# Kernel optimization log

Hardware: AMD Instinct MI355X
Metric: run time of the kernel (lower is better)

## Reference

```python
import jax, jax.numpy as jnp
import numpy as np

IN_FEAT = 256
HIDDEN = [512, 512]
DENSE = 512
BATCH, SEQ = 64, 1024


def setup_inputs() -> dict:
    key = jax.random.key(0)
    ks = jax.random.split(key, 16)
    d = {"x": jax.random.normal(ks[0], (BATCH, SEQ, IN_FEAT), dtype=jnp.float32)}
    in_dim = IN_FEAT
    ki = 1
    for li, h in enumerate(HIDDEN):
        # packed input kernel [in,3h] (r,z,n), input bias [3h], packed hidden kernel [h,3h], hn bias [h]
        d[f"W_i{li}"] = jax.random.normal(ks[ki], (in_dim, 3 * h), dtype=jnp.float32) / np.sqrt(in_dim); ki += 1
        d[f"b_i{li}"] = jnp.zeros((3 * h,), dtype=jnp.float32)
        d[f"W_h{li}"] = jax.random.normal(ks[ki], (h, 3 * h), dtype=jnp.float32) / np.sqrt(h); ki += 1
        d[f"b_hn{li}"] = jnp.zeros((h,), dtype=jnp.float32)
        in_dim = h
    d["W_out"] = jax.random.normal(ks[ki], (in_dim, DENSE), dtype=jnp.float32) / np.sqrt(in_dim)
    d["b_out"] = jnp.zeros((DENSE,), dtype=jnp.float32)
    return d


def _gru_layer(x, W_i, b_i, W_h, b_hn):
    """x: [B,T,D]. Flax GRUCell math: r,z gates sigmoid; n tanh with r-gated hidden path (hn has its own bias)."""
    B, T, _ = x.shape
    H = W_h.shape[0]
    # precompute all input-side gate projections once: [B,T,3H]
    xg = jnp.einsum('btd,dg->btg', x, W_i) + b_i

    def step(h, xg_t):
        hg = h @ W_h                              # [B,3H]
        xr, xz, xn = jnp.split(xg_t, 3, axis=-1)
        hr, hz, hn = jnp.split(hg, 3, axis=-1)
        r = jax.nn.sigmoid(xr + hr)
        z = jax.nn.sigmoid(xz + hz)
        n = jnp.tanh(xn + r * (hn + b_hn))
        h_new = (1.0 - z) * n + z * h
        return h_new, h_new

    h0 = jnp.zeros((B, H), x.dtype)
    hT, ys = jax.lax.scan(step, h0, jnp.swapaxes(xg, 0, 1))  # ys: [T,B,H]
    return hT, jnp.swapaxes(ys, 0, 1)


def reference(x, W_i0, b_i0, W_h0, b_hn0, W_i1, b_i1, W_h1, b_hn1, W_out, b_out):
    act = jnp.tanh
    c0, y = _gru_layer(x, W_i0, b_i0, W_h0, b_hn0)
    y = act(y)
    c1, y = _gru_layer(y, W_i1, b_i1, W_h1, b_hn1)
    y = act(y)
    out = act(y[:, -1, :] @ W_out + b_out)
    return (out, c0, c1)
```

## Files before the change

kernel.cpp:

```cpp
#include <hip/hip_runtime.h>


#define T_STEPS 1024
#define NWG_L0  32
#define NWG_TOT 64

typedef _Float16 f16x8 __attribute__((ext_vector_type(8)));
typedef float    f32x4 __attribute__((ext_vector_type(4)));

#define H0_OFF   0
#define H1_OFF   131072
#define Y0_OFF   262144
#define FLAG_OFF 393216
#define FSTRIDE  32

#define BUD_BAR  (1ull << 22)

#define WAITV0()   asm volatile("s_waitcnt vmcnt(0)")
#define SB()       __builtin_amdgcn_sched_barrier(0)
#define FENCE_VM() asm volatile("s_waitcnt vmcnt(0)" ::: "memory")

__device__ __forceinline__ float sigm_f(float x) { return 1.0f / (1.0f + __expf(-x)); }
__device__ __forceinline__ float tanh_f(float x) { return 2.0f / (1.0f + __expf(-2.0f * x)) - 1.0f; }

__device__ __forceinline__ f32x4 mfma16(f16x8 a, f16x8 b, f32x4 c) {
    return __builtin_amdgcn_mfma_f32_16x16x32_f16(a, b, c, 0, 0, 0);
}

__device__ __forceinline__ f16x8 pack8(const float* __restrict__ src, int stride) {
    f16x8 r;
#pragma unroll
    for (int j = 0; j < 8; ++j) r[j] = (_Float16)src[j * stride];
    return r;
}

__device__ __forceinline__ f16x8 ld_frag_a(const _Float16* p) {
    f16x8 v;
    asm volatile("global_load_dwordx4 %0, %1, off sc1" : "=v"(v) : "v"(p));
    return v;
}

__device__ __forceinline__ void st_dev_f16(_Float16* p, float v) {
    unsigned short b = __builtin_bit_cast(unsigned short, (_Float16)v);
    __hip_atomic_store((unsigned short*)p, b, __ATOMIC_RELAXED, __HIP_MEMORY_SCOPE_AGENT);
}

__device__ __forceinline__ void bar_arrive(unsigned* flags, int wg, unsigned epoch) {
    asm volatile("s_waitcnt vmcnt(0)" ::: "memory");
    __syncthreads();
    if (threadIdx.x == 0)
        __hip_atomic_store(&flags[wg * FSTRIDE], epoch,
                           __ATOMIC_RELAXED, __HIP_MEMORY_SCOPE_AGENT);
}
__device__ __forceinline__ void bar_wait_wd(const unsigned* flags, unsigned epoch,
                                            int wave, int lane,
                                            volatile unsigned* s_alive) {
    if (wave == 0 && *s_alive) {
        const unsigned* p = &flags[lane * FSTRIDE];
        unsigned long long t0 = clock64();
        for (;;) {
            unsigned v = __hip_atomic_load(p, __ATOMIC_RELAXED, __HIP_MEMORY_SCOPE_AGENT);
            if (__all(v >= epoch)) break;
            if (clock64() - t0 > BUD_BAR) { if (lane == 0) *s_alive = 0; break; }
        }
    }
    __syncthreads();
    asm volatile("" ::: "memory");
}

#define BFRAG(g, kt) __builtin_bit_cast(f16x8, ldsB[((g) * 16 + (kt)) * 64 + lane])

__global__ __launch_bounds__(256, 1) void gru_scan(
    const float* __restrict__ x,
    const float* __restrict__ Wi0,
    const float* __restrict__ bi0,
    const float* __restrict__ Wh0,
    const float* __restrict__ bhn0,
    const float* __restrict__ Wi1,
    const float* __restrict__ bi1,
    const float* __restrict__ Wh1,
    const float* __restrict__ bhn1,
    float* __restrict__ c0_out,
    float* __restrict__ c1_out,
    unsigned char* __restrict__ ws)
{
    __shared__ uint4 ldsB[48 * 64];
    __shared__ unsigned s_alive;

    const int tid  = threadIdx.x;
    const int wave = tid >> 6;
    const int lane = tid & 63;
    const int quad = lane >> 4;
    const int l16  = lane & 15;
    const int wg   = blockIdx.x;
    const bool isL1 = (wg >= NWG_L0);
    const int cslice = (isL1 ? (wg - NWG_L0) : wg) * 16;

    if (tid == 0) s_alive = 1u;

    _Float16* h0buf = (_Float16*)(ws + H0_OFF);
    _Float16* h1buf = (_Float16*)(ws + H1_OFF);
    _Float16* y0buf = (_Float16*)(ws + Y0_OFF);
    unsigned* flags = (unsigned*)(ws + FLAG_OFF);

    const float* Wh = isL1 ? Wh1 : Wh0;
    const float* Wi = isL1 ? Wi1 : Wi0;

    for (int f = wave * 12; f < wave * 12 + 12; ++f) {
        int nt = f >> 4, kt = f & 15;
        const float* src = Wh + (kt * 32 + quad * 8) * 1536 + nt * 512 + cslice + l16;
        ldsB[f * 64 + lane] = __builtin_bit_cast(uint4, pack8(src, 1536));
    }

    f16x8 wif[48];
    if (!isL1) {
#pragma unroll
        for (int nt = 0; nt < 3; ++nt)
#pragma unroll
            for (int kt = 0; kt < 8; ++kt)
                wif[nt * 8 + kt] = pack8(Wi + (kt * 32 + quad * 8) * 1536 + nt * 512 + cslice + l16, 1536);
    } else {
#pragma unroll
        for (int nt = 0; nt < 3; ++nt)
#pragma unroll
            for (int kt = 0; kt < 16; ++kt)
                wif[nt * 16 + kt] = pack8(Wi + (kt * 32 + quad * 8) * 1536 + nt * 512 + cslice + l16, 1536);
    }

    const float* bi = isL1 ? bi1 : bi0;
    const float* bh = isL1 ? bhn1 : bhn0;
    const float bi_r = bi[cslice + l16];
    const float bi_z = bi[512 + cslice + l16];
    const float bi_n = bi[1024 + cslice + l16];
    const float bhn  = bh[cslice + l16];

    __syncthreads();

    float hstate[4] = {0.f, 0.f, 0.f, 0.f};
    const int rowA = wave * 16 + l16;
    const int rowC = wave * 16 + quad * 4;
    const int cu   = cslice + l16;
    const f32x4 z4 = {0.f, 0.f, 0.f, 0.f};

    for (int s = 0; s < T_STEPS + 1; ++s) {
        const int pr = s & 1;

        f32x4 xr[16];
        if (!isL1 && s < T_STEPS) {
            const float* px = x + (size_t)rowA * 262144 + s * 256 + quad * 8;
#pragma unroll
            for (int kt = 0; kt < 8; ++kt) {
                xr[kt * 2]     = *(const f32x4*)(px + kt * 32);
                xr[kt * 2 + 1] = *(const f32x4*)(px + kt * 32 + 4);
            }
        }

        if (s > 0) bar_wait_wd(flags, (unsigned)s, wave, lane, &s_alive);

        if (!isL1 && s < T_STEPS) {
            const _Float16* hR = h0buf + pr * 32768;
            _Float16* hW = h0buf + (pr ^ 1) * 32768;
            _Float16* yW = y0buf + (pr ^ 1) * 32768;

            FENCE_VM();

            f16x8 axf[8];
#pragma unroll
            for (int kt = 0; kt < 8; ++kt) {
                f32x4 x0 = xr[kt * 2], x1 = xr[kt * 2 + 1];
                f16x8 a;
                a[0] = (_Float16)x0[0]; a[1] = (_Float16)x0[1];
                a[2] = (_Float16)x0[2]; a[3] = (_Float16)x0[3];
                a[4] = (_Float16)x1[0]; a[5] = (_Float16)x1[1];
                a[6] = (_Float16)x1[2]; a[7] = (_Float16)x1[3];
                axf[kt] = a;
            }
            SB();

            f16x8 hb[16];
#pragma unroll
            for (int p = 0; p < 16; ++p)
                hb[p] = ld_frag_a(hR + rowA * 512 + p * 32 + quad * 8);

            f32x4 ax0 = z4, ax1 = z4, ax2 = z4;
#pragma unroll
            for (int kt = 0; kt < 8; ++kt) {
                ax0 = mfma16(axf[kt], wif[0 * 8 + kt], ax0);
                ax1 = mfma16(axf[kt], wif[1 * 8 + kt], ax1);
                ax2 = mfma16(axf[kt], wif[2 * 8 + kt], ax2);
            }

            SB(); WAITV0(); SB();

            f32x4 ah0 = z4, ah1 = z4, ah2 = z4;
#pragma unroll
            for (int kt = 0; kt < 16; ++kt) {
                f16x8 a = hb[kt];
                ah0 = mfma16(a, BFRAG(0, kt), ah0);
                ah1 = mfma16(a, BFRAG(1, kt), ah1);
                ah2 = mfma16(a, BFRAG(2, kt), ah2);
            }

#pragma unroll
            for (int i = 0; i < 4; ++i) {
                const int b = rowC + i;
                float r = sigm_f(ax0[i] + bi_r + ah0[i]);
                float z = sigm_f(ax1[i] + bi_z + ah1[i]);
                float n = tanh_f(ax2[i] + bi_n + r * (ah2[i] + bhn));
                float hnew = (1.0f - z) * n + z * hstate[i];
                hstate[i] = hnew;
                st_dev_f16(&hW[b * 512 + cu], hnew);
                st_dev_f16(&yW[b * 512 + cu], tanh_f(hnew));
                if (s == T_STEPS - 1) c0_out[b * 512 + cu] = hnew;
            }
        }

        if (isL1 && s >= 1) {
            const _Float16* hR = h1buf + pr * 32768;
            _Float16* hW = h1buf + (pr ^ 1) * 32768;
            const _Float16* yR = y0buf + pr * 32768;

            FENCE_VM();
            SB();

            f16x8 hb[8], yb[8];
#pragma unroll
            for (int p = 0; p < 8; ++p) {
                hb[p] = ld_frag_a(hR + rowA * 512 + p * 32 + quad * 8);
                yb[p] = ld_frag_a(yR + rowA * 512 + p * 32 + quad * 8);
            }

            SB(); WAITV0(); SB();

            f32x4 ah0 = z4, ah1 = z4, ah2 = z4, ax0 = z4, ax1 = z4, ax2 = z4;
#pragma unroll
            for (int kt = 0; kt < 8; ++kt) {
                f16x8 ah = hb[kt], ay = yb[kt];
                ah0 = mfma16(ah, BFRAG(0, kt), ah0);
                ah1 = mfma16(ah, BFRAG(1, kt), ah1);
                ah2 = mfma16(ah, BFRAG(2, kt), ah2);
                ax0 = mfma16(ay, wif[0 * 16 + kt], ax0);
                ax1 = mfma16(ay, wif[1 * 16 + kt], ax1);
                ax2 = mfma16(ay, wif[2 * 16 + kt], ax2);
                hb[kt] = ld_frag_a(hR + rowA * 512 + (kt + 8) * 32 + quad * 8);
                yb[kt] = ld_frag_a(yR + rowA * 512 + (kt + 8) * 32 + quad * 8);
            }

            SB(); WAITV0(); SB();

#pragma unroll
            for (int kt = 8; kt < 16; ++kt) {
                f16x8 ah = hb[kt - 8], ay = yb[kt - 8];
                ah0 = mfma16(ah, BFRAG(0, kt), ah0);
                ah1 = mfma16(ah, BFRAG(1, kt), ah1);
                ah2 = mfma16(ah, BFRAG(2, kt), ah2);
                ax0 = mfma16(ay, wif[0 * 16 + kt], ax0);
                ax1 = mfma16(ay, wif[1 * 16 + kt], ax1);
                ax2 = mfma16(ay, wif[2 * 16 + kt], ax2);
            }

#pragma unroll
            for (int i = 0; i < 4; ++i) {
                const int b = rowC + i;
                float r = sigm_f(ax0[i] + bi_r + ah0[i]);
                float z = sigm_f(ax1[i] + bi_z + ah1[i]);
                float n = tanh_f(ax2[i] + bi_n + r * (ah2[i] + bhn));
                float hnew = (1.0f - z) * n + z * hstate[i];
                hstate[i] = hnew;
                st_dev_f16(&hW[b * 512 + cu], hnew);
                if (s == T_STEPS) c1_out[b * 512 + cu] = hnew;
            }
        }

        if (s < T_STEPS) bar_arrive(flags, wg, (unsigned)(s + 1));
    }
}

__global__ __launch_bounds__(256) void dense_out(
    const float* __restrict__ c1, const float* __restrict__ Wout,
    const float* __restrict__ bout, float* __restrict__ out)
{
    __shared__ float a[512];
    const int b = blockIdx.x, tid = threadIdx.x;
    a[tid]       = tanh_f(c1[b * 512 + tid]);
    a[tid + 256] = tanh_f(c1[b * 512 + tid + 256]);
    __syncthreads();
    float acc0 = 0.f, acc1 = 0.f;
#pragma unroll 4
    for (int k = 0; k < 512; ++k) {
        const float av = a[k];
        acc0 += av * Wout[k * 512 + tid];
        acc1 += av * Wout[k * 512 + tid + 256];
    }
    out[b * 512 + tid]       = tanh_f(acc0 + bout[tid]);
    out[b * 512 + tid + 256] = tanh_f(acc1 + bout[tid + 256]);
}

extern "C" void kernel_launch(void* const* d_in, const int* in_sizes, int n_in,
                              void* d_out, int out_size, void* d_ws, size_t ws_size,
                              hipStream_t stream)
{
    const float* x    = (const float*)d_in[0];
    const float* Wi0  = (const float*)d_in[1];
    const float* bi0  = (const float*)d_in[2];
    const float* Wh0  = (const float*)d_in[3];
    const float* bhn0 = (const float*)d_in[4];
    const float* Wi1  = (const float*)d_in[5];
    const float* bi1  = (const float*)d_in[6];
    const float* Wh1  = (const float*)d_in[7];
    const float* bhn1 = (const float*)d_in[8];
    const float* Wout = (const float*)d_in[9];
    const float* bout = (const float*)d_in[10];
    float* out = (float*)d_out;
    unsigned char* ws = (unsigned char*)d_ws;

    hipMemsetAsync(ws, 0, FLAG_OFF + 8192, stream);

    gru_scan<<<NWG_TOT, 256, 0, stream>>>(x, Wi0, bi0, Wh0, bhn0,
                                          Wi1, bi1, Wh1, bhn1,
                                          out + 32768, out + 65536, ws);
    dense_out<<<64, 256, 0, stream>>>(out + 65536, Wout, bout, out);
}
```

Before: 7.300 ms.

## Replace global barrier with tagged hidden-state data flags and layer pipelining

Drops the all-workgroup per-step barrier. Each 32-bit hidden-state word now carries its step number in the upper half, so readers check validity straight from the data they load. Layer 0 and layer 1 are decoupled through per-rank y-ready and progress flags, and a triple-buffered y stream lives in the output buffer. Input weights move from registers to LDS. The aim is to remove barrier latency and let the two layers run skewed, but the scheme depends on subtle memory-ordering assumptions and doubles the size of hidden-state traffic.

```diff
diff --git a/kernel.cpp b/kernel.cpp
--- a/kernel.cpp
+++ b/kernel.cpp
@@ -8,17 +8,15 @@
 typedef _Float16 f16x8 __attribute__((ext_vector_type(8)));
 typedef float    f32x4 __attribute__((ext_vector_type(4)));
 
-#define H0_OFF   0
-#define H1_OFF   131072
-#define Y0_OFF   262144
-#define FLAG_OFF 393216
-#define FSTRIDE  32
-
-#define BUD_BAR  (1ull << 22)
-
-#define WAITV0()   asm volatile("s_waitcnt vmcnt(0)")
-#define SB()       __builtin_amdgcn_sched_barrier(0)
-#define FENCE_VM() asm volatile("s_waitcnt vmcnt(0)" ::: "memory")
+#define H0T_OFF   0u
+#define H1T_OFF   262144u
+#define YFLAG_OFF 524288u
+#define PROG_OFF  526336u
+#define WS_NEED   528384u
+#define FST       16
+
+#define BUD_SPIN (1ull << 19)
+#define BUD_EPI  (1ull << 22)
 
 __device__ __forceinline__ float sigm_f(float x) { return 1.0f / (1.0f + __expf(-x)); }
 __device__ __forceinline__ float tanh_f(float x) { return 2.0f / (1.0f + __expf(-2.0f * x)) - 1.0f; }
@@ -34,58 +32,161 @@
     return r;
 }
 
-__device__ __forceinline__ f16x8 ld_frag_a(const _Float16* p) {
-    f16x8 v;
-    asm volatile("global_load_dwordx4 %0, %1, off sc1" : "=v"(v) : "v"(p));
-    return v;
-}
-
-__device__ __forceinline__ void st_dev_f16(_Float16* p, float v) {
-    unsigned short b = __builtin_bit_cast(unsigned short, (_Float16)v);
-    __hip_atomic_store((unsigned short*)p, b, __ATOMIC_RELAXED, __HIP_MEMORY_SCOPE_AGENT);
-}
-
-__device__ __forceinline__ void bar_arrive(unsigned* flags, int wg, unsigned epoch) {
-    asm volatile("s_waitcnt vmcnt(0)" ::: "memory");
-    __syncthreads();
-    if (threadIdx.x == 0)
-        __hip_atomic_store(&flags[wg * FSTRIDE], epoch,
-                           __ATOMIC_RELAXED, __HIP_MEMORY_SCOPE_AGENT);
-}
-__device__ __forceinline__ void bar_wait_wd(const unsigned* flags, unsigned epoch,
-                                            int wave, int lane,
-                                            volatile unsigned* s_alive) {
-    if (wave == 0 && *s_alive) {
-        const unsigned* p = &flags[lane * FSTRIDE];
-        unsigned long long t0 = clock64();
-        for (;;) {
-            unsigned v = __hip_atomic_load(p, __ATOMIC_RELAXED, __HIP_MEMORY_SCOPE_AGENT);
-            if (__all(v >= epoch)) break;
-            if (clock64() - t0 > BUD_BAR) { if (lane == 0) *s_alive = 0; break; }
-        }
+#define LDH33(W, PV, HB, PP) \
+  asm volatile( \
+    "global_load_dwordx4 %0, %33, off sc1\n\t" \
+    "global_load_dwordx4 %1, %33, off offset:16 sc1\n\t" \
+    "global_load_dwordx4 %2, %33, off offset:128 sc1\n\t" \
+    "global_load_dwordx4 %3, %33, off offset:144 sc1\n\t" \
+    "global_load_dwordx4 %4, %33, off offset:256 sc1\n\t" \
+    "global_load_dwordx4 %5, %33, off offset:272 sc1\n\t" \
+    "global_load_dwordx4 %6, %33, off offset:384 sc1\n\t" \
+    "global_load_dwordx4 %7, %33, off offset:400 sc1\n\t" \
+    "global_load_dwordx4 %8, %33, off offset:512 sc1\n\t" \
+    "global_load_dwordx4 %9, %33, off offset:528 sc1\n\t" \
+    "global_load_dwordx4 %10, %33, off offset:640 sc1\n\t" \
+    "global_load_dwordx4 %11, %33, off offset:656 sc1\n\t" \
+    "global_load_dwordx4 %12, %33, off offset:768 sc1\n\t" \
+    "global_load_dwordx4 %13, %33, off offset:784 sc1\n\t" \
+    "global_load_dwordx4 %14, %33, off offset:896 sc1\n\t" \
+    "global_load_dwordx4 %15, %33, off offset:912 sc1\n\t" \
+    "global_load_dwordx4 %16, %33, off offset:1024 sc1\n\t" \
+    "global_load_dwordx4 %17, %33, off offset:1040 sc1\n\t" \
+    "global_load_dwordx4 %18, %33, off offset:1152 sc1\n\t" \
+    "global_load_dwordx4 %19, %33, off offset:1168 sc1\n\t" \
+    "global_load_dwordx4 %20, %33, off offset:1280 sc1\n\t" \
+    "global_load_dwordx4 %21, %33, off offset:1296 sc1\n\t" \
+    "global_load_dwordx4 %22, %33, off offset:1408 sc1\n\t" \
+    "global_load_dwordx4 %23, %33, off offset:1424 sc1\n\t" \
+    "global_load_dwordx4 %24, %33, off offset:1536 sc1\n\t" \
+    "global_load_dwordx4 %25, %33, off offset:1552 sc1\n\t" \
+    "global_load_dwordx4 %26, %33, off offset:1664 sc1\n\t" \
+    "global_load_dwordx4 %27, %33, off offset:1680 sc1\n\t" \
+    "global_load_dwordx4 %28, %33, off offset:1792 sc1\n\t" \
+    "global_load_dwordx4 %29, %33, off offset:1808 sc1\n\t" \
+    "global_load_dwordx4 %30, %33, off offset:1920 sc1\n\t" \
+    "global_load_dwordx4 %31, %33, off offset:1936 sc1\n\t" \
+    "global_load_dword   %32, %34, off sc1\n\t" \
+    "s_waitcnt vmcnt(0)" \
+    : "=&v"((W)[0]), "=&v"((W)[1]), "=&v"((W)[2]), "=&v"((W)[3]), \
+      "=&v"((W)[4]), "=&v"((W)[5]), "=&v"((W)[6]), "=&v"((W)[7]), \
+      "=&v"((W)[8]), "=&v"((W)[9]), "=&v"((W)[10]), "=&v"((W)[11]), \
+      "=&v"((W)[12]), "=&v"((W)[13]), "=&v"((W)[14]), "=&v"((W)[15]), \
+      "=&v"((W)[16]), "=&v"((W)[17]), "=&v"((W)[18]), "=&v"((W)[19]), \
+      "=&v"((W)[20]), "=&v"((W)[21]), "=&v"((W)[22]), "=&v"((W)[23]), \
+      "=&v"((W)[24]), "=&v"((W)[25]), "=&v"((W)[26]), "=&v"((W)[27]), \
+      "=&v"((W)[28]), "=&v"((W)[29]), "=&v"((W)[30]), "=&v"((W)[31]), \
+      "=&v"(PV) \
+    : "v"(HB), "v"(PP) \
+    : "memory")
+
+#define LDX16(W, B) \
+  asm volatile( \
+    "global_load_dwordx4 %0, %16, off\n\t" \
+    "global_load_dwordx4 %1, %16, off offset:16\n\t" \
+    "global_load_dwordx4 %2, %16, off offset:128\n\t" \
+    "global_load_dwordx4 %3, %16, off offset:144\n\t" \
+    "global_load_dwordx4 %4, %16, off offset:256\n\t" \
+    "global_load_dwordx4 %5, %16, off offset:272\n\t" \
+    "global_load_dwordx4 %6, %16, off offset:384\n\t" \
+    "global_load_dwordx4 %7, %16, off offset:400\n\t" \
+    "global_load_dwordx4 %8, %16, off offset:512\n\t" \
+    "global_load_dwordx4 %9, %16, off offset:528\n\t" \
+    "global_load_dwordx4 %10, %16, off offset:640\n\t" \
+    "global_load_dwordx4 %11, %16, off offset:656\n\t" \
+    "global_load_dwordx4 %12, %16, off offset:768\n\t" \
+    "global_load_dwordx4 %13, %16, off offset:784\n\t" \
+    "global_load_dwordx4 %14, %16, off offset:896\n\t" \
+    "global_load_dwordx4 %15, %16, off offset:912\n\t" \
+    "s_waitcnt vmcnt(0)" \
+    : "=&v"((W)[0]), "=&v"((W)[1]), "=&v"((W)[2]), "=&v"((W)[3]), \
+      "=&v"((W)[4]), "=&v"((W)[5]), "=&v"((W)[6]), "=&v"((W)[7]), \
+      "=&v"((W)[8]), "=&v"((W)[9]), "=&v"((W)[10]), "=&v"((W)[11]), \
+      "=&v"((W)[12]), "=&v"((W)[13]), "=&v"((W)[14]), "=&v"((W)[15]) \
+    : "v"(B) \
+    : "memory")
+
+#define LDY16(W, B) \
+  asm volatile( \
+    "global_load_dwordx4 %0, %16, off sc1\n\t" \
+    "global_load_dwordx4 %1, %16, off offset:64 sc1\n\t" \
+    "global_load_dwordx4 %2, %16, off offset:128 sc1\n\t" \
+    "global_load_dwordx4 %3, %16, off offset:192 sc1\n\t" \
+    "global_load_dwordx4 %4, %16, off offset:256 sc1\n\t" \
+    "global_load_dwordx4 %5, %16, off offset:320 sc1\n\t" \
+    "global_load_dwordx4 %6, %16, off offset:384 sc1\n\t" \
+    "global_load_dwordx4 %7, %16, off offset:448 sc1\n\t" \
+    "global_load_dwordx4 %8, %16, off offset:512 sc1\n\t" \
+    "global_load_dwordx4 %9, %16, off offset:576 sc1\n\t" \
+    "global_load_dwordx4 %10, %16, off offset:640 sc1\n\t" \
+    "global_load_dwordx4 %11, %16, off offset:704 sc1\n\t" \
+    "global_load_dwordx4 %12, %16, off offset:768 sc1\n\t" \
+    "global_load_dwordx4 %13, %16, off offset:832 sc1\n\t" \
+    "global_load_dwordx4 %14, %16, off offset:896 sc1\n\t" \
+    "global_load_dwordx4 %15, %16, off offset:960 sc1\n\t" \
+    "s_waitcnt vmcnt(0)" \
+    : "=&v"((W)[0]), "=&v"((W)[1]), "=&v"((W)[2]), "=&v"((W)[3]), \
+      "=&v"((W)[4]), "=&v"((W)[5]), "=&v"((W)[6]), "=&v"((W)[7]), \
+      "=&v"((W)[8]), "=&v"((W)[9]), "=&v"((W)[10]), "=&v"((W)[11]), \
+      "=&v"((W)[12]), "=&v"((W)[13]), "=&v"((W)[14]), "=&v"((W)[15]) \
+    : "v"(B) \
+    : "memory")
+
+__device__ __forceinline__ void st_u1_sc1(unsigned* p, unsigned v) {
+    asm volatile("global_store_dword %0, %1, off sc1" :: "v"(p), "v"(v) : "memory");
+}
+__device__ __forceinline__ void st_h_sc1(_Float16* p, float f) {
+    unsigned hv = (unsigned)__builtin_bit_cast(unsigned short, (_Float16)f);
+    asm volatile("global_store_short %0, %1, off sc1" :: "v"(p), "v"(hv) : "memory");
+}
+
+__device__ __forceinline__ void spin_ge(const unsigned* p, int tgt, bool* dead,
+                                        unsigned long long bud) {
+    if (*dead) return;
+    unsigned long long t0 = clock64();
+    for (;;) {
+        unsigned v;
+        asm volatile("global_load_dword %0, %1, off sc1\n\ts_waitcnt vmcnt(0)"
+                     : "=v"(v) : "v"(p) : "memory");
+        if (__all((int)v >= tgt)) return;
+        if (clock64() - t0 > bud) { *dead = true; return; }
     }
-    __syncthreads();
-    asm volatile("" ::: "memory");
+}
+
+__device__ __forceinline__ unsigned vb32(const uint4* w, unsigned etag) {
+    unsigned a = 0;
+#pragma unroll
+    for (int i = 0; i < 32; ++i)
+        a |= (w[i].x ^ etag) | (w[i].y ^ etag) | (w[i].z ^ etag) | (w[i].w ^ etag);
+    return a >> 16;
+}
+__device__ __forceinline__ f16x8 packfrag(uint4 lo, uint4 hi) {
+    uint4 r;
+    r.x = (lo.x & 0xFFFFu) | (lo.y << 16);
+    r.y = (lo.z & 0xFFFFu) | (lo.w << 16);
+    r.z = (hi.x & 0xFFFFu) | (hi.y << 16);
+    r.w = (hi.z & 0xFFFFu) | (hi.w << 16);
+    return __builtin_bit_cast(f16x8, r);
 }
 
 #define BFRAG(g, kt) __builtin_bit_cast(f16x8, ldsB[((g) * 16 + (kt)) * 64 + lane])
+#define WFRAG(g, kt) __builtin_bit_cast(f16x8, ldsWi[((g) * 16 + (kt)) * 64 + lane])
 
 __global__ __launch_bounds__(256, 1) void gru_scan(
     const float* __restrict__ x,
-    const float* __restrict__ Wi0,
-    const float* __restrict__ bi0,
-    const float* __restrict__ Wh0,
-    const float* __restrict__ bhn0,
-    const float* __restrict__ Wi1,
-    const float* __restrict__ bi1,
-    const float* __restrict__ Wh1,
-    const float* __restrict__ bhn1,
+    const float* __restrict__ Wi0, const float* __restrict__ bi0,
+    const float* __restrict__ Wh0, const float* __restrict__ bhn0,
+    const float* __restrict__ Wi1, const float* __restrict__ bi1,
+    const float* __restrict__ Wh1, const float* __restrict__ bhn1,
     float* __restrict__ c0_out,
     float* __restrict__ c1_out,
+    _Float16* __restrict__ y0p,
+    _Float16* __restrict__ y1p,
+    _Float16* __restrict__ y2p,
     unsigned char* __restrict__ ws)
 {
     __shared__ uint4 ldsB[48 * 64];
-    __shared__ unsigned s_alive;
+    __shared__ uint4 ldsWi[48 * 64];
 
     const int tid  = threadIdx.x;
     const int wave = tid >> 6;
@@ -94,14 +195,11 @@
     const int l16  = lane & 15;
     const int wg   = blockIdx.x;
     const bool isL1 = (wg >= NWG_L0);
-    const int cslice = (isL1 ? (wg - NWG_L0) : wg) * 16;
-
-    if (tid == 0) s_alive = 1u;
-
-    _Float16* h0buf = (_Float16*)(ws + H0_OFF);
-    _Float16* h1buf = (_Float16*)(ws + H1_OFF);
-    _Float16* y0buf = (_Float16*)(ws + Y0_OFF);
-    unsigned* flags = (unsigned*)(ws + FLAG_OFF);
+    const int rank = isL1 ? (wg - NWG_L0) : wg;
+    const int cslice = rank * 16;
+
+    unsigned* yfl  = (unsigned*)(ws + YFLAG_OFF);
+    unsigned* prog = (unsigned*)(ws + PROG_OFF);
 
     const float* Wh = isL1 ? Wh1 : Wh0;
     const float* Wi = isL1 ? Wi1 : Wi0;
@@ -110,21 +208,10 @@
         int nt = f >> 4, kt = f & 15;
         const float* src = Wh + (kt * 32 + quad * 8) * 1536 + nt * 512 + cslice + l16;
         ldsB[f * 64 + lane] = __builtin_bit_cast(uint4, pack8(src, 1536));
-    }
-
-    f16x8 wif[48];
-    if (!isL1) {
-#pragma unroll
-        for (int nt = 0; nt < 3; ++nt)
-#pragma unroll
-            for (int kt = 0; kt < 8; ++kt)
-                wif[nt * 8 + kt] = pack8(Wi + (kt * 32 + quad * 8) * 1536 + nt * 512 + cslice + l16, 1536);
-    } else {
-#pragma unroll
-        for (int nt = 0; nt < 3; ++nt)
-#pragma unroll
-            for (int kt = 0; kt < 16; ++kt)
-                wif[nt * 16 + kt] = pack8(Wi + (kt * 32 + quad * 8) * 1536 + nt * 512 + cslice + l16, 1536);
+        if (isL1 || kt < 8) {
+            const float* si = Wi + (kt * 32 + quad * 8) * 1536 + nt * 512 + cslice + l16;
+            ldsWi[f * 64 + lane] = __builtin_bit_cast(uint4, pack8(si, 1536));
+        }
     }
 
     const float* bi = isL1 ? bi1 : bi0;
@@ -141,138 +228,168 @@
     const int rowC = wave * 16 + quad * 4;
     const int cu   = cslice + l16;
     const f32x4 z4 = {0.f, 0.f, 0.f, 0.f};
-
-    for (int s = 0; s < T_STEPS + 1; ++s) {
-        const int pr = s & 1;
-
-        f32x4 xr[16];
-        if (!isL1 && s < T_STEPS) {
-            const float* px = x + (size_t)rowA * 262144 + s * 256 + quad * 8;
+    bool dead = false;
+
+    if (!isL1) {
+        unsigned* h0t = (unsigned*)(ws + H0T_OFF);
+        const unsigned* ppML = prog + (lane & 31) * FST;
+        unsigned* myyfl = yfl + rank * FST;
+        float c0st[4] = {0.f, 0.f, 0.f, 0.f};
+
+        for (int s = 0; s < T_STEPS; ++s) {
+            uint4 xw[16];
+            const float* xb = x + (size_t)rowA * 262144 + (size_t)s * 256 + quad * 8;
+            LDX16(xw, xb);
+
+            f32x4 ax0 = z4, ax1 = z4, ax2 = z4;
 #pragma unroll
             for (int kt = 0; kt < 8; ++kt) {
-                xr[kt * 2]     = *(const f32x4*)(px + kt * 32);
-                xr[kt * 2 + 1] = *(const f32x4*)(px + kt * 32 + 4);
-            }
-        }
-
-        if (s > 0) bar_wait_wd(flags, (unsigned)s, wave, lane, &s_alive);
-
-        if (!isL1 && s < T_STEPS) {
-            const _Float16* hR = h0buf + pr * 32768;
-            _Float16* hW = h0buf + (pr ^ 1) * 32768;
-            _Float16* yW = y0buf + (pr ^ 1) * 32768;
-
-            FENCE_VM();
-
-            f16x8 axf[8];
-#pragma unroll
-            for (int kt = 0; kt < 8; ++kt) {
-                f32x4 x0 = xr[kt * 2], x1 = xr[kt * 2 + 1];
+                f32x4 x0 = __builtin_bit_cast(f32x4, xw[2 * kt]);
+                f32x4 x1 = __builtin_bit_cast(f32x4, xw[2 * kt + 1]);
                 f16x8 a;
                 a[0] = (_Float16)x0[0]; a[1] = (_Float16)x0[1];
                 a[2] = (_Float16)x0[2]; a[3] = (_Float16)x0[3];
                 a[4] = (_Float16)x1[0]; a[5] = (_Float16)x1[1];
                 a[6] = (_Float16)x1[2]; a[7] = (_Float16)x1[3];
-                axf[kt] = a;
-            }
-            SB();
-
-            f16x8 hb[16];
-#pragma unroll
-            for (int p = 0; p < 16; ++p)
-                hb[p] = ld_frag_a(hR + rowA * 512 + p * 32 + quad * 8);
-
-            f32x4 ax0 = z4, ax1 = z4, ax2 = z4;
-#pragma unroll
-            for (int kt = 0; kt < 8; ++kt) {
-                ax0 = mfma16(axf[kt], wif[0 * 8 + kt], ax0);
-                ax1 = mfma16(axf[kt], wif[1 * 8 + kt], ax1);
-                ax2 = mfma16(axf[kt], wif[2 * 8 + kt], ax2);
-            }
-
-            SB(); WAITV0(); SB();
+                ax0 = mfma16(a, WFRAG(0, kt), ax0);
+                ax1 = mfma16(a, WFRAG(1, kt), ax1);
+                ax2 = mfma16(a, WFRAG(2, kt), ax2);
+            }
+
+            const unsigned etag = (unsigned)s << 16;
+            const unsigned* hbR = h0t + (unsigned)(s & 1) * 32768u + rowA * 512 + quad * 8;
+            uint4 w[32]; unsigned pv;
+            LDH33(w, pv, hbR, ppML);
+
+            __syncthreads();
+            if (tid == 0) st_u1_sc1(myyfl, (unsigned)s);
+
+            unsigned bad = vb32(w, etag);
+            if (__any((int)(bad != 0u)) && !dead) {
+                unsigned long long t0 = clock64();
+                while (__any((int)(bad != 0u))) {
+                    LDH33(w, pv, hbR, ppML);
+                    bad = vb32(w, etag);
+                    if (clock64() - t0 > BUD_SPIN) { dead = true; break; }
+                }
+            }
 
             f32x4 ah0 = z4, ah1 = z4, ah2 = z4;
 #pragma unroll
             for (int kt = 0; kt < 16; ++kt) {
-                f16x8 a = hb[kt];
+                f16x8 a = packfrag(w[2 * kt], w[2 * kt + 1]);
                 ah0 = mfma16(a, BFRAG(0, kt), ah0);
                 ah1 = mfma16(a, BFRAG(1, kt), ah1);
                 ah2 = mfma16(a, BFRAG(2, kt), ah2);
             }
 
+            float hnv[4], ytv[4];
 #pragma unroll
             for (int i = 0; i < 4; ++i) {
-                const int b = rowC + i;
-                float r = sigm_f(ax0[i] + bi_r + ah0[i]);
-                float z = sigm_f(ax1[i] + bi_z + ah1[i]);
-                float n = tanh_f(ax2[i] + bi_n + r * (ah2[i] + bhn));
-                float hnew = (1.0f - z) * n + z * hstate[i];
-                hstate[i] = hnew;
-                st_dev_f16(&hW[b * 512 + cu], hnew);
-                st_dev_f16(&yW[b * 512 + cu], tanh_f(hnew));
-                if (s == T_STEPS - 1) c0_out[b * 512 + cu] = hnew;
+                float r  = sigm_f(ax0[i] + bi_r + ah0[i]);
+                float zz = sigm_f(ax1[i] + bi_z + ah1[i]);
+                float n  = tanh_f(ax2[i] + bi_n + r * (ah2[i] + bhn));
+                float hnew = (1.0f - zz) * n + zz * hstate[i];
+                hstate[i] = hnew; hnv[i] = hnew; ytv[i] = tanh_f(hnew);
+            }
+
+            if (s >= 2 && !__all((int)pv >= s - 2))
+                spin_ge(ppML, s - 2, &dead, BUD_SPIN);
+
+            unsigned* hw = h0t + (unsigned)((s + 1) & 1) * 32768u;
+            const unsigned wtag = (unsigned)(s + 1) << 16;
+            const int sl = (s + 1) % 3;
+            _Float16* yw = (sl == 0) ? y0p : ((sl == 1) ? y1p : y2p);
+#pragma unroll
+            for (int i = 0; i < 4; ++i) {
+                unsigned hb16 = (unsigned)__builtin_bit_cast(unsigned short, (_Float16)hnv[i]);
+                st_u1_sc1(hw + (rowC + i) * 512 + cu, wtag | hb16);
+                st_h_sc1(yw + (rowC + i) * 512 + cu, ytv[i]);
+            }
+            if (s == T_STEPS - 1) {
+#pragma unroll
+                for (int i = 0; i < 4; ++i) c0st[i] = hnv[i];
             }
         }
 
-        if (isL1 && s >= 1) {
-            const _Float16* hR = h1buf + pr * 32768;
-            _Float16* hW = h1buf + (pr ^ 1) * 32768;
-            const _Float16* yR = y0buf + pr * 32768;
-
-            FENCE_VM();
-            SB();
-
-            f16x8 hb[8], yb[8];
-#pragma unroll
-            for (int p = 0; p < 8; ++p) {
-                hb[p] = ld_frag_a(hR + rowA * 512 + p * 32 + quad * 8);
-                yb[p] = ld_frag_a(yR + rowA * 512 + p * 32 + quad * 8);
-            }
-
-            SB(); WAITV0(); SB();
-
-            f32x4 ah0 = z4, ah1 = z4, ah2 = z4, ax0 = z4, ax1 = z4, ax2 = z4;
-#pragma unroll
-            for (int kt = 0; kt < 8; ++kt) {
-                f16x8 ah = hb[kt], ay = yb[kt];
-                ah0 = mfma16(ah, BFRAG(0, kt), ah0);
-                ah1 = mfma16(ah, BFRAG(1, kt), ah1);
-                ah2 = mfma16(ah, BFRAG(2, kt), ah2);
-                ax0 = mfma16(ay, wif[0 * 16 + kt], ax0);
-                ax1 = mfma16(ay, wif[1 * 16 + kt], ax1);
-                ax2 = mfma16(ay, wif[2 * 16 + kt], ax2);
-                hb[kt] = ld_frag_a(hR + rowA * 512 + (kt + 8) * 32 + quad * 8);
-                yb[kt] = ld_frag_a(yR + rowA * 512 + (kt + 8) * 32 + quad * 8);
-            }
-
-            SB(); WAITV0(); SB();
-
-#pragma unroll
-            for (int kt = 8; kt < 16; ++kt) {
-                f16x8 ah = hb[kt - 8], ay = yb[kt - 8];
-                ah0 = mfma16(ah, BFRAG(0, kt), ah0);
-                ah1 = mfma16(ah, BFRAG(1, kt), ah1);
-                ah2 = mfma16(ah, BFRAG(2, kt), ah2);
-                ax0 = mfma16(ay, wif[0 * 16 + kt], ax0);
-                ax1 = mfma16(ay, wif[1 * 16 + kt], ax1);
-                ax2 = mfma16(ay, wif[2 * 16 + kt], ax2);
-            }
-
+        asm volatile("s_waitcnt vmcnt(0)" ::: "memory");
+        __syncthreads();
+        if (tid == 0) st_u1_sc1(myyfl, (unsigned)T_STEPS);
+        spin_ge(ppML, 1022, &dead, BUD_EPI);
+#pragma unroll
+        for (int i = 0; i < 4; ++i)
+            c0_out[(rowC + i) * 512 + cu] = c0st[i];
+
+    } else {
+        unsigned* h1t = (unsigned*)(ws + H1T_OFF);
+        const unsigned* ppYF = yfl + (lane & 31) * FST;
+        unsigned* myprog = prog + rank * FST;
+
+        for (int s = 1; s <= T_STEPS; ++s) {
+            const unsigned etag = (unsigned)(s - 1) << 16;
+            const unsigned* hbR = h1t + (unsigned)((s - 1) & 1) * 32768u + rowA * 512 + quad * 8;
+            uint4 w[32]; unsigned yv;
+            LDH33(w, yv, hbR, ppYF);
+
+            if (!__all((int)yv >= s))
+                spin_ge(ppYF, s, &dead, BUD_SPIN);
+
+            const int sl = s % 3;
+            const _Float16* yb_ = ((sl == 0) ? y0p : ((sl == 1) ? y1p : y2p))
+                                  + rowA * 512 + quad * 8;
+            uint4 yw16[16];
+            LDY16(yw16, yb_);
+
+            f32x4 ax0 = z4, ax1 = z4, ax2 = z4;
+#pragma unroll
+            for (int kt = 0; kt < 16; ++kt) {
+                f16x8 ay = __builtin_bit_cast(f16x8, yw16[kt]);
+                ax0 = mfma16(ay, WFRAG(0, kt), ax0);
+                ax1 = mfma16(ay, WFRAG(1, kt), ax1);
+                ax2 = mfma16(ay, WFRAG(2, kt), ax2);
+            }
+
+            unsigned bad = vb32(w, etag);
+            if (__any((int)(bad != 0u)) && !dead) {
+                unsigned long long t0 = clock64();
+                while (__any((int)(bad != 0u))) {
+                    LDH33(w, yv, hbR, ppYF);
+                    bad = vb32(w, etag);
+                    if (clock64() - t0 > BUD_SPIN) { dead = true; break; }
+                }
+            }
+
+            f32x4 ah0 = z4, ah1 = z4, ah2 = z4;
+#pragma unroll
+            for (int kt = 0; kt < 16; ++kt) {
+                f16x8 a = packfrag(w[2 * kt], w[2 * kt + 1]);
+                ah0 = mfma16(a, BFRAG(0, kt), ah0);
+                ah1 = mfma16(a, BFRAG(1, kt), ah1);
+                ah2 = mfma16(a, BFRAG(2, kt), ah2);
+            }
+
+            float hnv[4];
 #pragma unroll
             for (int i = 0; i < 4; ++i) {
-                const int b = rowC + i;
-                float r = sigm_f(ax0[i] + bi_r + ah0[i]);
-                float z = sigm_f(ax1[i] + bi_z + ah1[i]);
-                float n = tanh_f(ax2[i] + bi_n + r * (ah2[i] + bhn));
-                float hnew = (1.0f - z) * n + z * hstate[i];
-                hstate[i] = hnew;
-                st_dev_f16(&hW[b * 512 + cu], hnew);
-                if (s == T_STEPS) c1_out[b * 512 + cu] = hnew;
-            }
+                float r  = sigm_f(ax0[i] + bi_r + ah0[i]);
+                float zz = sigm_f(ax1[i] + bi_z + ah1[i]);
+                float n  = tanh_f(ax2[i] + bi_n + r * (ah2[i] + bhn));
+                float hnew = (1.0f - zz) * n + zz * hstate[i];
+                hstate[i] = hnew; hnv[i] = hnew;
+            }
+
+            unsigned* hw = h1t + (unsigned)(s & 1) * 32768u;
+            const unsigned wtag = (unsigned)s << 16;
+#pragma unroll
+            for (int i = 0; i < 4; ++i) {
+                unsigned hb16 = (unsigned)__builtin_bit_cast(unsigned short, (_Float16)hnv[i]);
+                st_u1_sc1(hw + (rowC + i) * 512 + cu, wtag | hb16);
+                if (s == T_STEPS) c1_out[(rowC + i) * 512 + cu] = hnv[i];
+            }
+
+            __syncthreads();
+            if (tid == 0) st_u1_sc1(myprog, (unsigned)s);
         }
-
-        if (s < T_STEPS) bar_arrive(flags, wg, (unsigned)(s + 1));
     }
 }
 
@@ -314,10 +431,16 @@
     float* out = (float*)d_out;
     unsigned char* ws = (unsigned char*)d_ws;
 
-    hipMemsetAsync(ws, 0, FLAG_OFF + 8192, stream);
+    float* c0 = out + 32768;
+    float* c1 = out + 65536;
+    _Float16* y0p = (_Float16*)out;
+    _Float16* y1p = y0p + 32768;
+    _Float16* y2p = (_Float16*)c0;
+
+    hipMemsetAsync(ws, 0, WS_NEED, stream);
 
     gru_scan<<<NWG_TOT, 256, 0, stream>>>(x, Wi0, bi0, Wh0, bhn0,
                                           Wi1, bi1, Wh1, bhn1,
-                                          out + 32768, out + 65536, ws);
-    dense_out<<<64, 256, 0, stream>>>(out + 65536, Wout, bout, out);
-}
+                                          c0, c1, y0p, y1p, y2p, ws);
+    dense_out<<<64, 256, 0, stream>>>(c1, Wout, bout, out);
+}
```

Result: slower. 10.28 ms (+40.8%).
